# Kernel tuning notes

Hardware: AMD Instinct MI355X
Metric: run time of the kernel (lower is better)

## Reference

```python
import jax, jax.numpy as jnp
import numpy as np

N = 50000        # nodes
E = 800000       # edges (avg degree 16)
G = 64           # graphs in batch
F_IN = 9
OUT = 10


def setup_inputs() -> dict:
    key = jax.random.key(0)
    ks = jax.random.split(key, 20)
    def w(k, fi, fo):
        return jax.random.normal(k, (fi, fo), dtype=jnp.float32) * (1.0 / np.sqrt(fi))
    inp = {
        "x": jax.random.normal(ks[0], (N, F_IN), dtype=jnp.float32),
        "edge_index": jax.random.randint(ks[1], (2, E), 0, N, dtype=jnp.int64),
        "batch": jnp.sort(jax.random.randint(ks[2], (N,), 0, G, dtype=jnp.int64)),
        # GCNConv weights (PyG: x @ W then normalized scatter-add, + bias)
        "W1": w(ks[3], F_IN, 128), "b1": jnp.zeros((128,), jnp.float32),
        "W2": w(ks[4], 128, 256),  "b2": jnp.zeros((256,), jnp.float32),
        "W3": w(ks[5], 256, 256),  "b3": jnp.zeros((256,), jnp.float32),
        "W4": w(ks[6], 256, 256),  "b4": jnp.zeros((256,), jnp.float32),
        # dense head
        "Wl2": w(ks[7], 256, 128), "bl2": jnp.zeros((128,), jnp.float32),
        "Wl3": w(ks[8], 128, 128), "bl3": jnp.zeros((128,), jnp.float32),
        "Wl":  w(ks[9], 128, OUT), "bl":  jnp.zeros((OUT,), jnp.float32),
    }
    return inp


def reference(x, edge_index, batch, W1, b1, W2, b2, W3, b3, W4, b4,
              Wl2, bl2, Wl3, bl3, Wl, bl):
    # GCNConv with self-loops and symmetric deg^{-1/2} normalization
    loops = jnp.arange(N, dtype=edge_index.dtype)
    src = jnp.concatenate([edge_index[0], loops])   # [E+N]
    dst = jnp.concatenate([edge_index[1], loops])
    deg = jax.ops.segment_sum(jnp.ones_like(src, dtype=x.dtype), dst, num_segments=N)
    dinv = jax.lax.rsqrt(deg)                        # deg >= 1 due to self-loops
    norm = (dinv[src] * dinv[dst])[:, None]          # [E+N, 1]

    def conv(h, W, b):
        msg = (h @ W)[src] * norm                    # gather + normalize
        return jax.ops.segment_sum(msg, dst, num_segments=N) + b

    h = jax.nn.relu(conv(x, W1, b1))
    h = jax.nn.relu(conv(h, W2, b2))
    h = jax.nn.relu(conv(h, W3, b3))
    h = conv(h, W4, b4)                              # no relu before pool
    g = jax.ops.segment_max(h, batch, num_segments=G)  # global_max_pool -> [G, 256]
    g = jax.nn.relu(g @ Wl2 + bl2)
    g = jax.nn.relu(g @ Wl3 + bl3)
    out = g @ Wl + bl                                # [G, OUT]
    return jnp.squeeze(out)
```

## Files before the change

kernel.cpp:

```cpp
#include <hip/hip_runtime.h>
#include <float.h>

#define NN 50000
#define NE 800000
#define NG 64
#define CAP 64

typedef __attribute__((ext_vector_type(8))) _Float16 f16x8;
typedef __attribute__((ext_vector_type(4))) float f32x4;
typedef __attribute__((ext_vector_type(4))) _Float16 half4;
typedef __attribute__((ext_vector_type(2))) _Float16 half2v;
typedef unsigned int u32;
typedef unsigned short u16;

__device__ __forceinline__ unsigned f2mono(float f) {
  unsigned b = __float_as_uint(f);
  return (b & 0x80000000u) ? ~b : (b | 0x80000000u);
}
__device__ __forceinline__ float mono2f(unsigned u) {
  unsigned b = (u & 0x80000000u) ? (u & 0x7fffffffu) : ~u;
  return __uint_as_float(b);
}
__device__ __forceinline__ void gl_lds16(const void* g, void* l) {
  __builtin_amdgcn_global_load_lds((const __attribute__((address_space(1))) u32*)g,
                                   (__attribute__((address_space(3))) u32*)l, 16, 0, 0);
}

__global__ void k_count(const int* __restrict__ src, const int* __restrict__ dst,
                        int* __restrict__ cnt, u16* __restrict__ col) {
  int e = blockIdx.x * 256 + threadIdx.x;
  if (e >= NE) return;
  int d = dst[e];
  int s = src[e];
  if ((unsigned)d >= NN || (unsigned)s >= NN) return;
  int pos = atomicAdd(&cnt[d], 1);
  if (pos < CAP) col[d * CAP + pos] = (u16)s;
}

__global__ void k_dinv(const int* __restrict__ cnt, float* __restrict__ dinv,
                       const float* __restrict__ x, float* __restrict__ xs,
                       unsigned* __restrict__ g) {
  int v = blockIdx.x * blockDim.x + threadIdx.x;
  if (v >= NN) return;
  if (v < NG * 256) g[v] = 0u;
  float d = rsqrtf((float)cnt[v] + 1.0f);
  dinv[v] = d;
#pragma unroll
  for (int i = 0; i < 9; ++i) xs[v * 9 + i] = x[v * 9 + i] * d;
}

__device__ __forceinline__ void splitw1(const float* W, _Float16* Wh, _Float16* Wl,
                                        int i, int K, int Nc) {
  int k = i / Nc, n = i - k * Nc;
  float w = W[i];
  _Float16 h = (_Float16)w;
  _Float16 l = (_Float16)(w - (float)h);
  Wh[(size_t)n * K + k] = h;
  Wl[(size_t)n * K + k] = l;
}
__global__ void k_splitw3(const float* __restrict__ W2, const float* __restrict__ W3,
                          const float* __restrict__ W4,
                          _Float16* __restrict__ W2h, _Float16* __restrict__ W2l,
                          _Float16* __restrict__ W3h, _Float16* __restrict__ W3l,
                          _Float16* __restrict__ W4h, _Float16* __restrict__ W4l) {
  int i = blockIdx.x * 256 + threadIdx.x;
  const int n2 = 128 * 256, n3 = 256 * 256;
  if (i < n2) splitw1(W2, W2h, W2l, i, 128, 256);
  else if (i < n2 + n3) splitw1(W3, W3h, W3l, i - n2, 256, 256);
  else if (i < n2 + 2 * n3) splitw1(W4, W4h, W4l, i - n2 - n3, 256, 256);
}

__global__ __launch_bounds__(256) void k_agg9(const float* __restrict__ xs,
                                              float* __restrict__ out,
                                              const int* __restrict__ cnt,
                                              const u16* __restrict__ col,
                                              const float* __restrict__ dinv) {
  int v = (blockIdx.x * 256 + threadIdx.x) >> 4;
  int l = threadIdx.x & 15;
  if (v >= NN) return;
  int c = cnt[v]; if (c > CAP) c = CAP;
  const u16* cl = col + (size_t)v * CAP;
  float acc = (l < 9) ? xs[v * 9 + l] : 0.0f;
  int j = 0;
  for (; j + 4 <= c; j += 4) {
    ushort4 u = *(const ushort4*)(cl + j);
    float a0 = (l < 9) ? xs[(int)u.x * 9 + l] : 0.f;
    float a1 = (l < 9) ? xs[(int)u.y * 9 + l] : 0.f;
    float a2 = (l < 9) ? xs[(int)u.z * 9 + l] : 0.f;
    float a3 = (l < 9) ? xs[(int)u.w * 9 + l] : 0.f;
    acc += (a0 + a1) + (a2 + a3);
  }
  for (; j < c; ++j) {
    int u = cl[j];
    if (l < 9) acc += xs[u * 9 + l];
  }
  if (l < 9) out[v * 9 + l] = acc * dinv[v];
}

__global__ __launch_bounds__(256) void k_gemm9(const float* __restrict__ in,
                                               const float* __restrict__ W,
                                               const float* __restrict__ bias,
                                               const float* __restrict__ dinv,
                                               _Float16* __restrict__ out) {
  __shared__ float sW[9 * 128];
  __shared__ float sb[128];
  int t = threadIdx.x;
  if (t < 128) sb[t] = bias[t];
  for (int i = t; i < 9 * 128; i += 256) sW[i] = W[i];
  __syncthreads();
  int r = blockIdx.x * 2 + (t >> 7);
  int c = t & 127;
  if (r >= NN) return;
  float acc = sb[c];
#pragma unroll
  for (int i = 0; i < 9; ++i) acc += in[r * 9 + i] * sW[i * 128 + c];
  out[r * 128 + c] = (_Float16)(fmaxf(acc, 0.0f) * dinv[r]);
}

__global__ __launch_bounds__(256) void k_agg128(const half2v* __restrict__ h,
                                                half2v* __restrict__ out,
                                                const int* __restrict__ cnt,
                                                const u16* __restrict__ col,
                                                const float* __restrict__ dinv) {
  int gw = (blockIdx.x * 256 + threadIdx.x) >> 6;
  int lane = threadIdx.x & 63;
  int w0 = gw * 2, w1 = w0 + 1;
  if (w0 >= NN) return;
  half2v s0 = h[(size_t)w0 * 64 + lane];
  half2v s1 = h[(size_t)w1 * 64 + lane];
  float a0x = (float)s0.x, a0y = (float)s0.y;
  float a1x = (float)s1.x, a1y = (float)s1.y;
  int c0 = cnt[w0]; if (c0 > CAP) c0 = CAP;
  int c1 = cnt[w1]; if (c1 > CAP) c1 = CAP;
  const u16* cl0 = col + (size_t)w0 * CAP;
  const u16* cl1 = col + (size_t)w1 * CAP;
  int j0 = 0, j1 = 0;
  while (j0 + 4 <= c0 && j1 + 4 <= c1) {
    ushort4 u0 = *(const ushort4*)(cl0 + j0);
    ushort4 u1 = *(const ushort4*)(cl1 + j1);
    half2v t00 = h[(size_t)u0.x * 64 + lane];
    half2v t01 = h[(size_t)u0.y * 64 + lane];
    half2v t02 = h[(size_t)u0.z * 64 + lane];
    half2v t03 = h[(size_t)u0.w * 64 + lane];
    half2v t10 = h[(size_t)u1.x * 64 + lane];
    half2v t11 = h[(size_t)u1.y * 64 + lane];
    half2v t12 = h[(size_t)u1.z * 64 + lane];
    half2v t13 = h[(size_t)u1.w * 64 + lane];
    a0x += ((float)t00.x + (float)t01.x) + ((float)t02.x + (float)t03.x);
    a0y += ((float)t00.y + (float)t01.y) + ((float)t02.y + (float)t03.y);
    a1x += ((float)t10.x + (float)t11.x) + ((float)t12.x + (float)t13.x);
    a1y += ((float)t10.y + (float)t11.y) + ((float)t12.y + (float)t13.y);
    j0 += 4; j1 += 4;
  }
  for (; j0 + 4 <= c0; j0 += 4) {
    ushort4 u = *(const ushort4*)(cl0 + j0);
    half2v t0 = h[(size_t)u.x * 64 + lane];
    half2v t1 = h[(size_t)u.y * 64 + lane];
    half2v t2 = h[(size_t)u.z * 64 + lane];
    half2v t3 = h[(size_t)u.w * 64 + lane];
    a0x += ((float)t0.x + (float)t1.x) + ((float)t2.x + (float)t3.x);
    a0y += ((float)t0.y + (float)t1.y) + ((float)t2.y + (float)t3.y);
  }
  for (; j1 + 4 <= c1; j1 += 4) {
    ushort4 u = *(const ushort4*)(cl1 + j1);
    half2v t0 = h[(size_t)u.x * 64 + lane];
    half2v t1 = h[(size_t)u.y * 64 + lane];
    half2v t2 = h[(size_t)u.z * 64 + lane];
    half2v t3 = h[(size_t)u.w * 64 + lane];
    a1x += ((float)t0.x + (float)t1.x) + ((float)t2.x + (float)t3.x);
    a1y += ((float)t0.y + (float)t1.y) + ((float)t2.y + (float)t3.y);
  }
  for (; j0 < c0; ++j0) {
    half2v tv = h[(size_t)cl0[j0] * 64 + lane];
    a0x += (float)tv.x; a0y += (float)tv.y;
  }
  for (; j1 < c1; ++j1) {
    half2v tv = h[(size_t)cl1[j1] * 64 + lane];
    a1x += (float)tv.x; a1y += (float)tv.y;
  }
  float d0 = dinv[w0], d1 = dinv[w1];
  half2v o0, o1;
  o0.x = (_Float16)(a0x * d0); o0.y = (_Float16)(a0y * d0);
  o1.x = (_Float16)(a1x * d1); o1.y = (_Float16)(a1y * d1);
  out[(size_t)w0 * 64 + lane] = o0;
  out[(size_t)w1 * 64 + lane] = o1;
}

__global__ __launch_bounds__(256) void k_agg256(const half4* __restrict__ h,
                                                half4* __restrict__ out,
                                                const int* __restrict__ cnt,
                                                const u16* __restrict__ col,
                                                const float* __restrict__ dinv) {
  int gw = (blockIdx.x * 256 + threadIdx.x) >> 6;
  int lane = threadIdx.x & 63;
  int w0 = gw * 2, w1 = w0 + 1;
  if (w0 >= NN) return;
  half4 s0 = h[(size_t)w0 * 64 + lane];
  half4 s1 = h[(size_t)w1 * 64 + lane];
  float a0x = (float)s0.x, a0y = (float)s0.y, a0z = (float)s0.z, a0w = (float)s0.w;
  float a1x = (float)s1.x, a1y = (float)s1.y, a1z = (float)s1.z, a1w = (float)s1.w;
  int c0 = cnt[w0]; if (c0 > CAP) c0 = CAP;
  int c1 = cnt[w1]; if (c1 > CAP) c1 = CAP;
  const u16* cl0 = col + (size_t)w0 * CAP;
  const u16* cl1 = col + (size_t)w1 * CAP;
  int j0 = 0, j1 = 0;
  while (j0 + 4 <= c0 && j1 + 4 <= c1) {
    ushort4 u0 = *(const ushort4*)(cl0 + j0);
    ushort4 u1 = *(const ushort4*)(cl1 + j1);
    half4 t00 = h[(size_t)u0.x * 64 + lane];
    half4 t01 = h[(size_t)u0.y * 64 + lane];
    half4 t02 = h[(size_t)u0.z * 64 + lane];
    half4 t03 = h[(size_t)u0.w * 64 + lane];
    half4 t10 = h[(size_t)u1.x * 64 + lane];
    half4 t11 = h[(size_t)u1.y * 64 + lane];
    half4 t12 = h[(size_t)u1.z * 64 + lane];
    half4 t13 = h[(size_t)u1.w * 64 + lane];
    a0x += ((float)t00.x + (float)t01.x) + ((float)t02.x + (float)t03.x);
    a0y += ((float)t00.y + (float)t01.y) + ((float)t02.y + (float)t03.y);
    a0z += ((float)t00.z + (float)t01.z) + ((float)t02.z + (float)t03.z);
    a0w += ((float)t00.w + (float)t01.w) + ((float)t02.w + (float)t03.w);
    a1x += ((float)t10.x + (float)t11.x) + ((float)t12.x + (float)t13.x);
    a1y += ((float)t10.y + (float)t11.y) + ((float)t12.y + (float)t13.y);
    a1z += ((float)t10.z + (float)t11.z) + ((float)t12.z + (float)t13.z);
    a1w += ((float)t10.w + (float)t11.w) + ((float)t12.w + (float)t13.w);
    j0 += 4; j1 += 4;
  }
  for (; j0 + 4 <= c0; j0 += 4) {
    ushort4 u = *(const ushort4*)(cl0 + j0);
    half4 t0 = h[(size_t)u.x * 64 + lane];
    half4 t1 = h[(size_t)u.y * 64 + lane];
    half4 t2 = h[(size_t)u.z * 64 + lane];
    half4 t3 = h[(size_t)u.w * 64 + lane];
    a0x += ((float)t0.x + (float)t1.x) + ((float)t2.x + (float)t3.x);
    a0y += ((float)t0.y + (float)t1.y) + ((float)t2.y + (float)t3.y);
    a0z += ((float)t0.z + (float)t1.z) + ((float)t2.z + (float)t3.z);
    a0w += ((float)t0.w + (float)t1.w) + ((float)t2.w + (float)t3.w);
  }
  for (; j1 + 4 <= c1; j1 += 4) {
    ushort4 u = *(const ushort4*)(cl1 + j1);
    half4 t0 = h[(size_t)u.x * 64 + lane];
    half4 t1 = h[(size_t)u.y * 64 + lane];
    half4 t2 = h[(size_t)u.z * 64 + lane];
    half4 t3 = h[(size_t)u.w * 64 + lane];
    a1x += ((float)t0.x + (float)t1.x) + ((float)t2.x + (float)t3.x);
    a1y += ((float)t0.y + (float)t1.y) + ((float)t2.y + (float)t3.y);
    a1z += ((float)t0.z + (float)t1.z) + ((float)t2.z + (float)t3.z);
    a1w += ((float)t0.w + (float)t1.w) + ((float)t2.w + (float)t3.w);
  }
  for (; j0 < c0; ++j0) {
    half4 tv = h[(size_t)cl0[j0] * 64 + lane];
    a0x += (float)tv.x; a0y += (float)tv.y; a0z += (float)tv.z; a0w += (float)tv.w;
  }
  for (; j1 < c1; ++j1) {
    half4 tv = h[(size_t)cl1[j1] * 64 + lane];
    a1x += (float)tv.x; a1y += (float)tv.y; a1z += (float)tv.z; a1w += (float)tv.w;
  }
  float d0 = dinv[w0], d1 = dinv[w1];
  half4 o0, o1;
  o0.x = (_Float16)(a0x * d0); o0.y = (_Float16)(a0y * d0);
  o0.z = (_Float16)(a0z * d0); o0.w = (_Float16)(a0w * d0);
  o1.x = (_Float16)(a1x * d1); o1.y = (_Float16)(a1y * d1);
  o1.z = (_Float16)(a1z * d1); o1.w = (_Float16)(a1w * d1);
  out[(size_t)w0 * 64 + lane] = o0;
  out[(size_t)w1 * 64 + lane] = o1;
}

__global__ __launch_bounds__(256) void k_mm(const _Float16* __restrict__ A,
                                            const _Float16* __restrict__ Bh,
                                            const _Float16* __restrict__ Bl,
                                            const float* __restrict__ bias,
                                            _Float16* __restrict__ C,
                                            const float* __restrict__ dinv,
                                            const int* __restrict__ batch,
                                            unsigned* __restrict__ gpool,
                                            int M, int K, int Nc, int mode) {
  __shared__ __align__(16) _Float16 Alds[128 * 64];
  __shared__ __align__(16) _Float16 Bhl[128 * 64];
  __shared__ __align__(16) _Float16 Bll[128 * 64];
  int bid = blockIdx.x;
  int rblk = (bid >> 4) * 8 + (bid & 7);
  int cblk = (bid >> 3) & 1;
  if (rblk * 128 >= M) return;
  int rowBase = rblk * 128;
  int colBase = cblk * 128;
  int t = threadIdx.x;
  int wave = t >> 6, lane = t & 63;
  int wm = wave & 1, wn = wave >> 1;
  int lm = lane & 15;
  int q  = lane >> 4;

  int srl = wave * 32 + (lane >> 3);
  int sj  = lane & 7;
  int ssw = lane >> 3;
  int gseg = sj ^ ssw;

  f32x4 acc[4][4];
#pragma unroll
  for (int i = 0; i < 4; ++i)
#pragma unroll
    for (int j = 0; j < 4; ++j) acc[i][j] = (f32x4){0.f, 0.f, 0.f, 0.f};

  int nit = K >> 6;
  for (int it = 0; it < nit; ++it) {
    __syncthreads();
#pragma unroll
    for (int c = 0; c < 4; ++c) {
      int rl = srl + c * 8;
      int ga = rowBase + rl; if (ga > M - 1) ga = M - 1;
      int gb = colBase + rl;
      unsigned off = (unsigned)it * 64 + gseg * 8;
      int ldst = (wave * 32 + c * 8) * 64 + lane * 8;
      gl_lds16(A  + (size_t)ga * K + off, Alds + ldst);
      gl_lds16(Bh + (size_t)gb * K + off, Bhl + ldst);
      gl_lds16(Bl + (size_t)gb * K + off, Bll + ldst);
    }
    __syncthreads();

#pragma unroll
    for (int s2 = 0; s2 < 2; ++s2) {
      int slotq = ((s2 << 2) | q);
      f16x8 vbh[4], vbl[4];
#pragma unroll
      for (int ni = 0; ni < 4; ++ni) {
        int rB = wn * 64 + ni * 16 + lm;
        int slot = slotq ^ (lm & 7);
        vbh[ni] = *(const f16x8*)(Bhl + rB * 64 + slot * 8);
        vbl[ni] = *(const f16x8*)(Bll + rB * 64 + slot * 8);
      }
#pragma unroll
      for (int mi = 0; mi < 4; ++mi) {
        int rA = wm * 64 + mi * 16 + lm;
        int slot = slotq ^ (lm & 7);
        f16x8 va = *(const f16x8*)(Alds + rA * 64 + slot * 8);
#pragma unroll
        for (int ni = 0; ni < 4; ++ni) {
          acc[mi][ni] = __builtin_amdgcn_mfma_f32_16x16x32_f16(va, vbh[ni], acc[mi][ni], 0, 0, 0);
          acc[mi][ni] = __builtin_amdgcn_mfma_f32_16x16x32_f16(va, vbl[ni], acc[mi][ni], 0, 0, 0);
        }
      }
    }
  }

  int rowOff = (lane >> 4) * 4;
  if (mode == 2) {
    __syncthreads();
    unsigned* ldsPool = (unsigned*)Alds;
    for (int i = t; i < 4 * 256; i += 256) ldsPool[i] = 0u;
    __syncthreads();
    int b0 = batch[rowBase];
#pragma unroll
    for (int mi = 0; mi < 4; ++mi) {
#pragma unroll
      for (int ni = 0; ni < 4; ++ni) {
        int gc = colBase + wn * 64 + ni * 16 + lm;
        float bsv = bias[gc];
#pragma unroll
        for (int r = 0; r < 4; ++r) {
          int gr = rowBase + wm * 64 + mi * 16 + rowOff + r;
          if (gr < M) {
            float v = acc[mi][ni][r] + bsv;
            int idx = batch[gr] - b0;
            if (idx < 0) idx = 0;
            if (idx > 3) idx = 3;
            atomicMax(&ldsPool[idx * 256 + gc], f2mono(v));
          }
        }
      }
    }
    __syncthreads();
#pragma unroll
    for (int s4 = 0; s4 < 4; ++s4) {
      unsigned mv = ldsPool[s4 * 256 + t];
      int gb = b0 + s4;
      if (mv && gb < NG) atomicMax(&gpool[gb * 256 + t], mv);
    }
  } else {
#pragma unroll
    for (int mi = 0; mi < 4; ++mi) {
#pragma unroll
      for (int ni = 0; ni < 4; ++ni) {
        int gc = colBase + wn * 64 + ni * 16 + lm;
        float bsv = bias[gc];
#pragma unroll
        for (int r = 0; r < 4; ++r) {
          int gr = rowBase + wm * 64 + mi * 16 + rowOff + r;
          if (gr < M) {
            float v = fmaxf(acc[mi][ni][r] + bsv, 0.0f);
            C[(size_t)gr * Nc + gc] = (_Float16)(v * dinv[gr]);
          }
        }
      }
    }
  }
}

__global__ __launch_bounds__(256) void k_head(const unsigned* __restrict__ g,
                                              const float* __restrict__ Wl2, const float* __restrict__ bl2,
                                              const float* __restrict__ Wl3, const float* __restrict__ bl3,
                                              const float* __restrict__ Wl, const float* __restrict__ bl,
                                              float* __restrict__ out) {
  __shared__ float s0[256];
  __shared__ float s1[128];
  __shared__ float s2[128];
  int b = blockIdx.x, t = threadIdx.x;
  s0[t] = mono2f(g[b * 256 + t]);
  __syncthreads();
  if (t < 128) {
    float acc = bl2[t];
    for (int k = 0; k < 256; ++k) acc += s0[k] * Wl2[k * 128 + t];
    s1[t] = fmaxf(acc, 0.0f);
  }
  __syncthreads();
  if (t < 128) {
    float acc = bl3[t];
    for (int k = 0; k < 128; ++k) acc += s1[k] * Wl3[k * 128 + t];
    s2[t] = fmaxf(acc, 0.0f);
  }
  __syncthreads();
  if (t < 10) {
    float acc = bl[t];
    for (int k = 0; k < 128; ++k) acc += s2[k] * Wl[k * 10 + t];
    out[b * 10 + t] = acc;
  }
}

extern "C" void kernel_launch(void* const* d_in, const int* in_sizes, int n_in,
                              void* d_out, int out_size, void* d_ws, size_t ws_size,
                              hipStream_t stream) {
  const float* x   = (const float*)d_in[0];
  const int* eidx  = (const int*)d_in[1];
  const int* batch = (const int*)d_in[2];
  const float* W1 = (const float*)d_in[3];   const float* b1 = (const float*)d_in[4];
  const float* W2 = (const float*)d_in[5];   const float* b2 = (const float*)d_in[6];
  const float* W3 = (const float*)d_in[7];   const float* b3 = (const float*)d_in[8];
  const float* W4 = (const float*)d_in[9];   const float* b4 = (const float*)d_in[10];
  const float* Wl2 = (const float*)d_in[11]; const float* bl2 = (const float*)d_in[12];
  const float* Wl3 = (const float*)d_in[13]; const float* bl3 = (const float*)d_in[14];
  const float* Wl  = (const float*)d_in[15]; const float* bl  = (const float*)d_in[16];
  float* out = (float*)d_out;

  _Float16* bufA = (_Float16*)d_ws;
  _Float16* bufB = bufA + (size_t)NN * 256;
  int* cnt  = (int*)(bufB + (size_t)NN * 256);
  float* dinv = (float*)(cnt + NN);
  u16* col  = (u16*)(dinv + NN);
  unsigned* g = (unsigned*)(col + (size_t)NN * CAP);
  _Float16* W2h = (_Float16*)(g + NG * 256);
  _Float16* W2l = W2h + 256 * 128;
  _Float16* W3h = W2l + 256 * 128;
  _Float16* W3l = W3h + 256 * 256;
  _Float16* W4h = W3l + 256 * 256;
  _Float16* W4l = W4h + 256 * 256;
  float* xs = (float*)bufA;
  float* agg9out = (float*)bufB;

  const int* src = eidx;
  const int* dst = eidx + NE;

  hipMemsetAsync(cnt, 0, NN * sizeof(int), stream);

  k_count<<<(NE + 255) / 256, 256, 0, stream>>>(src, dst, cnt, col);
  k_dinv<<<(NN + 255) / 256, 256, 0, stream>>>(cnt, dinv, x, xs, g);

  k_splitw3<<<(128 * 256 + 2 * 256 * 256 + 255) / 256, 256, 0, stream>>>(
      W2, W3, W4, W2h, W2l, W3h, W3l, W4h, W4l);

  k_agg9<<<(NN + 15) / 16, 256, 0, stream>>>(xs, agg9out, cnt, col, dinv);
  k_gemm9<<<NN / 2, 256, 0, stream>>>(agg9out, W1, b1, dinv, bufA);

  int aggGrid = ((NN / 2) * 64 + 255) / 256;
  const int mmGrid = 784;

  k_agg128<<<aggGrid, 256, 0, stream>>>((const half2v*)bufA, (half2v*)bufB, cnt, col, dinv);
  k_mm<<<mmGrid, 256, 0, stream>>>(bufB, W2h, W2l, b2, bufA, dinv, batch, g, NN, 128, 256, 1);

  k_agg256<<<aggGrid, 256, 0, stream>>>((const half4*)bufA, (half4*)bufB, cnt, col, dinv);
  k_mm<<<mmGrid, 256, 0, stream>>>(bufB, W3h, W3l, b3, bufA, dinv, batch, g, NN, 256, 256, 1);

  k_agg256<<<aggGrid, 256, 0, stream>>>((const half4*)bufA, (half4*)bufB, cnt, col, dinv);
  k_mm<<<mmGrid, 256, 0, stream>>>(bufB, W4h, W4l, b4, bufA, dinv, batch, g, NN, 256, 256, 2);

  k_head<<<NG, 256, 0, stream>>>(g, Wl2, bl2, Wl3, bl3, Wl, bl, out);
}
```

Baseline: 437.5 us.

## Replace per-wave aggregation with feature-sliced 16-lane node groups

```diff
diff --git a/kernel.cpp b/kernel.cpp
--- a/kernel.cpp
+++ b/kernel.cpp
@@ -9,7 +9,6 @@
 typedef __attribute__((ext_vector_type(8))) _Float16 f16x8;
 typedef __attribute__((ext_vector_type(4))) float f32x4;
 typedef __attribute__((ext_vector_type(4))) _Float16 half4;
-typedef __attribute__((ext_vector_type(2))) _Float16 half2v;
 typedef unsigned int u32;
 typedef unsigned short u16;
 
@@ -117,152 +116,45 @@
   out[r * 128 + c] = (_Float16)(fmaxf(acc, 0.0f) * dinv[r]);
 }
 
-__global__ __launch_bounds__(256) void k_agg128(const half2v* __restrict__ h,
-                                                half2v* __restrict__ out,
-                                                const int* __restrict__ cnt,
-                                                const u16* __restrict__ col,
-                                                const float* __restrict__ dinv) {
-  int gw = (blockIdx.x * 256 + threadIdx.x) >> 6;
-  int lane = threadIdx.x & 63;
-  int w0 = gw * 2, w1 = w0 + 1;
-  if (w0 >= NN) return;
-  half2v s0 = h[(size_t)w0 * 64 + lane];
-  half2v s1 = h[(size_t)w1 * 64 + lane];
-  float a0x = (float)s0.x, a0y = (float)s0.y;
-  float a1x = (float)s1.x, a1y = (float)s1.y;
-  int c0 = cnt[w0]; if (c0 > CAP) c0 = CAP;
-  int c1 = cnt[w1]; if (c1 > CAP) c1 = CAP;
-  const u16* cl0 = col + (size_t)w0 * CAP;
-  const u16* cl1 = col + (size_t)w1 * CAP;
-  int j0 = 0, j1 = 0;
-  while (j0 + 4 <= c0 && j1 + 4 <= c1) {
-    ushort4 u0 = *(const ushort4*)(cl0 + j0);
-    ushort4 u1 = *(const ushort4*)(cl1 + j1);
-    half2v t00 = h[(size_t)u0.x * 64 + lane];
-    half2v t01 = h[(size_t)u0.y * 64 + lane];
-    half2v t02 = h[(size_t)u0.z * 64 + lane];
-    half2v t03 = h[(size_t)u0.w * 64 + lane];
-    half2v t10 = h[(size_t)u1.x * 64 + lane];
-    half2v t11 = h[(size_t)u1.y * 64 + lane];
-    half2v t12 = h[(size_t)u1.z * 64 + lane];
-    half2v t13 = h[(size_t)u1.w * 64 + lane];
-    a0x += ((float)t00.x + (float)t01.x) + ((float)t02.x + (float)t03.x);
-    a0y += ((float)t00.y + (float)t01.y) + ((float)t02.y + (float)t03.y);
-    a1x += ((float)t10.x + (float)t11.x) + ((float)t12.x + (float)t13.x);
-    a1y += ((float)t10.y + (float)t11.y) + ((float)t12.y + (float)t13.y);
-    j0 += 4; j1 += 4;
-  }
-  for (; j0 + 4 <= c0; j0 += 4) {
-    ushort4 u = *(const ushort4*)(cl0 + j0);
-    half2v t0 = h[(size_t)u.x * 64 + lane];
-    half2v t1 = h[(size_t)u.y * 64 + lane];
-    half2v t2 = h[(size_t)u.z * 64 + lane];
-    half2v t3 = h[(size_t)u.w * 64 + lane];
-    a0x += ((float)t0.x + (float)t1.x) + ((float)t2.x + (float)t3.x);
-    a0y += ((float)t0.y + (float)t1.y) + ((float)t2.y + (float)t3.y);
-  }
-  for (; j1 + 4 <= c1; j1 += 4) {
-    ushort4 u = *(const ushort4*)(cl1 + j1);
-    half2v t0 = h[(size_t)u.x * 64 + lane];
-    half2v t1 = h[(size_t)u.y * 64 + lane];
-    half2v t2 = h[(size_t)u.z * 64 + lane];
-    half2v t3 = h[(size_t)u.w * 64 + lane];
-    a1x += ((float)t0.x + (float)t1.x) + ((float)t2.x + (float)t3.x);
-    a1y += ((float)t0.y + (float)t1.y) + ((float)t2.y + (float)t3.y);
-  }
-  for (; j0 < c0; ++j0) {
-    half2v tv = h[(size_t)cl0[j0] * 64 + lane];
-    a0x += (float)tv.x; a0y += (float)tv.y;
-  }
-  for (; j1 < c1; ++j1) {
-    half2v tv = h[(size_t)cl1[j1] * 64 + lane];
-    a1x += (float)tv.x; a1y += (float)tv.y;
-  }
-  float d0 = dinv[w0], d1 = dinv[w1];
-  half2v o0, o1;
-  o0.x = (_Float16)(a0x * d0); o0.y = (_Float16)(a0y * d0);
-  o1.x = (_Float16)(a1x * d1); o1.y = (_Float16)(a1y * d1);
-  out[(size_t)w0 * 64 + lane] = o0;
-  out[(size_t)w1 * 64 + lane] = o1;
-}
-
-__global__ __launch_bounds__(256) void k_agg256(const half4* __restrict__ h,
-                                                half4* __restrict__ out,
-                                                const int* __restrict__ cnt,
-                                                const u16* __restrict__ col,
-                                                const float* __restrict__ dinv) {
-  int gw = (blockIdx.x * 256 + threadIdx.x) >> 6;
-  int lane = threadIdx.x & 63;
-  int w0 = gw * 2, w1 = w0 + 1;
-  if (w0 >= NN) return;
-  half4 s0 = h[(size_t)w0 * 64 + lane];
-  half4 s1 = h[(size_t)w1 * 64 + lane];
-  float a0x = (float)s0.x, a0y = (float)s0.y, a0z = (float)s0.z, a0w = (float)s0.w;
-  float a1x = (float)s1.x, a1y = (float)s1.y, a1z = (float)s1.z, a1w = (float)s1.w;
-  int c0 = cnt[w0]; if (c0 > CAP) c0 = CAP;
-  int c1 = cnt[w1]; if (c1 > CAP) c1 = CAP;
-  const u16* cl0 = col + (size_t)w0 * CAP;
-  const u16* cl1 = col + (size_t)w1 * CAP;
-  int j0 = 0, j1 = 0;
-  while (j0 + 4 <= c0 && j1 + 4 <= c1) {
-    ushort4 u0 = *(const ushort4*)(cl0 + j0);
-    ushort4 u1 = *(const ushort4*)(cl1 + j1);
-    half4 t00 = h[(size_t)u0.x * 64 + lane];
-    half4 t01 = h[(size_t)u0.y * 64 + lane];
-    half4 t02 = h[(size_t)u0.z * 64 + lane];
-    half4 t03 = h[(size_t)u0.w * 64 + lane];
-    half4 t10 = h[(size_t)u1.x * 64 + lane];
-    half4 t11 = h[(size_t)u1.y * 64 + lane];
-    half4 t12 = h[(size_t)u1.z * 64 + lane];
-    half4 t13 = h[(size_t)u1.w * 64 + lane];
-    a0x += ((float)t00.x + (float)t01.x) + ((float)t02.x + (float)t03.x);
-    a0y += ((float)t00.y + (float)t01.y) + ((float)t02.y + (float)t03.y);
-    a0z += ((float)t00.z + (float)t01.z) + ((float)t02.z + (float)t03.z);
-    a0w += ((float)t00.w + (float)t01.w) + ((float)t02.w + (float)t03.w);
-    a1x += ((float)t10.x + (float)t11.x) + ((float)t12.x + (float)t13.x);
-    a1y += ((float)t10.y + (float)t11.y) + ((float)t12.y + (float)t13.y);
-    a1z += ((float)t10.z + (float)t11.z) + ((float)t12.z + (float)t13.z);
-    a1w += ((float)t10.w + (float)t11.w) + ((float)t12.w + (float)t13.w);
-    j0 += 4; j1 += 4;
-  }
-  for (; j0 + 4 <= c0; j0 += 4) {
-    ushort4 u = *(const ushort4*)(cl0 + j0);
-    half4 t0 = h[(size_t)u.x * 64 + lane];
-    half4 t1 = h[(size_t)u.y * 64 + lane];
-    half4 t2 = h[(size_t)u.z * 64 + lane];
-    half4 t3 = h[(size_t)u.w * 64 + lane];
-    a0x += ((float)t0.x + (float)t1.x) + ((float)t2.x + (float)t3.x);
-    a0y += ((float)t0.y + (float)t1.y) + ((float)t2.y + (float)t3.y);
-    a0z += ((float)t0.z + (float)t1.z) + ((float)t2.z + (float)t3.z);
-    a0w += ((float)t0.w + (float)t1.w) + ((float)t2.w + (float)t3.w);
-  }
-  for (; j1 + 4 <= c1; j1 += 4) {
-    ushort4 u = *(const ushort4*)(cl1 + j1);
-    half4 t0 = h[(size_t)u.x * 64 + lane];
-    half4 t1 = h[(size_t)u.y * 64 + lane];
-    half4 t2 = h[(size_t)u.z * 64 + lane];
-    half4 t3 = h[(size_t)u.w * 64 + lane];
-    a1x += ((float)t0.x + (float)t1.x) + ((float)t2.x + (float)t3.x);
-    a1y += ((float)t0.y + (float)t1.y) + ((float)t2.y + (float)t3.y);
-    a1z += ((float)t0.z + (float)t1.z) + ((float)t2.z + (float)t3.z);
-    a1w += ((float)t0.w + (float)t1.w) + ((float)t2.w + (float)t3.w);
-  }
-  for (; j0 < c0; ++j0) {
-    half4 tv = h[(size_t)cl0[j0] * 64 + lane];
-    a0x += (float)tv.x; a0y += (float)tv.y; a0z += (float)tv.z; a0w += (float)tv.w;
-  }
-  for (; j1 < c1; ++j1) {
-    half4 tv = h[(size_t)cl1[j1] * 64 + lane];
-    a1x += (float)tv.x; a1y += (float)tv.y; a1z += (float)tv.z; a1w += (float)tv.w;
-  }
-  float d0 = dinv[w0], d1 = dinv[w1];
-  half4 o0, o1;
-  o0.x = (_Float16)(a0x * d0); o0.y = (_Float16)(a0y * d0);
-  o0.z = (_Float16)(a0z * d0); o0.w = (_Float16)(a0w * d0);
-  o1.x = (_Float16)(a1x * d1); o1.y = (_Float16)(a1y * d1);
-  o1.z = (_Float16)(a1z * d1); o1.w = (_Float16)(a1w * d1);
-  out[(size_t)w0 * 64 + lane] = o0;
-  out[(size_t)w1 * 64 + lane] = o1;
+__global__ __launch_bounds__(256) void k_aggs(const half4* __restrict__ h,
+                                              half4* __restrict__ out,
+                                              const int* __restrict__ cnt,
+                                              const u16* __restrict__ col,
+                                              const float* __restrict__ dinv,
+                                              int rowU, int slog) {
+  int bid = blockIdx.x;
+  int s = bid & ((1 << slog) - 1);
+  int chunk = bid >> slog;
+  int g = threadIdx.x >> 4;
+  int l = threadIdx.x & 15;
+  int v = chunk * 16 + g;
+  if (v >= NN) return;
+  int so = s * 16 + l;
+  int c = cnt[v]; if (c > CAP) c = CAP;
+  const u16* cl = col + (size_t)v * CAP;
+  half4 sv = h[(size_t)v * rowU + so];
+  float ax = (float)sv.x, ay = (float)sv.y, az = (float)sv.z, aw = (float)sv.w;
+  int j = 0;
+  for (; j + 4 <= c; j += 4) {
+    ushort4 u = *(const ushort4*)(cl + j);
+    half4 t0 = h[(size_t)u.x * rowU + so];
+    half4 t1 = h[(size_t)u.y * rowU + so];
+    half4 t2 = h[(size_t)u.z * rowU + so];
+    half4 t3 = h[(size_t)u.w * rowU + so];
+    ax += ((float)t0.x + (float)t1.x) + ((float)t2.x + (float)t3.x);
+    ay += ((float)t0.y + (float)t1.y) + ((float)t2.y + (float)t3.y);
+    az += ((float)t0.z + (float)t1.z) + ((float)t2.z + (float)t3.z);
+    aw += ((float)t0.w + (float)t1.w) + ((float)t2.w + (float)t3.w);
+  }
+  for (; j < c; ++j) {
+    half4 tv = h[(size_t)cl[j] * rowU + so];
+    ax += (float)tv.x; ay += (float)tv.y; az += (float)tv.z; aw += (float)tv.w;
+  }
+  float d = dinv[v];
+  half4 o;
+  o.x = (_Float16)(ax * d); o.y = (_Float16)(ay * d);
+  o.z = (_Float16)(az * d); o.w = (_Float16)(aw * d);
+  out[(size_t)v * rowU + so] = o;
 }
 
 __global__ __launch_bounds__(256) void k_mm(const _Float16* __restrict__ A,
@@ -468,16 +360,16 @@
   k_agg9<<<(NN + 15) / 16, 256, 0, stream>>>(xs, agg9out, cnt, col, dinv);
   k_gemm9<<<NN / 2, 256, 0, stream>>>(agg9out, W1, b1, dinv, bufA);
 
-  int aggGrid = ((NN / 2) * 64 + 255) / 256;
+  const int nchunk = (NN + 15) / 16;
   const int mmGrid = 784;
 
-  k_agg128<<<aggGrid, 256, 0, stream>>>((const half2v*)bufA, (half2v*)bufB, cnt, col, dinv);
+  k_aggs<<<nchunk * 2, 256, 0, stream>>>((const half4*)bufA, (half4*)bufB, cnt, col, dinv, 32, 1);
   k_mm<<<mmGrid, 256, 0, stream>>>(bufB, W2h, W2l, b2, bufA, dinv, batch, g, NN, 128, 256, 1);
 
-  k_agg256<<<aggGrid, 256, 0, stream>>>((const half4*)bufA, (half4*)bufB, cnt, col, dinv);
+  k_aggs<<<nchunk * 4, 256, 0, stream>>>((const half4*)bufA, (half4*)bufB, cnt, col, dinv, 64, 2);
   k_mm<<<mmGrid, 256, 0, stream>>>(bufB, W3h, W3l, b3, bufA, dinv, batch, g, NN, 256, 256, 1);
 
-  k_agg256<<<aggGrid, 256, 0, stream>>>((const half4*)bufA, (half4*)bufB, cnt, col, dinv);
+  k_aggs<<<nchunk * 4, 256, 0, stream>>>((const half4*)bufA, (half4*)bufB, cnt, col, dinv, 64, 2);
   k_mm<<<mmGrid, 256, 0, stream>>>(bufB, W4h, W4l, b4, bufA, dinv, batch, g, NN, 256, 256, 2);
 
   k_head<<<NG, 256, 0, stream>>>(g, Wl2, bl2, Wl3, bl3, Wl, bl, out);
```

Measured after the change: 439.6 us. Within noise of the previous version (+0.5%).
